# Kernel tuning notes

Hardware: AMD Instinct MI355X
Metric: run time of the kernel (lower is better)

The kernel has to match this reference:

```python
import jax, jax.numpy as jnp
import numpy as np
import math

N_COMP = 8          # config.project.shape[1]
REG_TOPK = 4        # config.reg_topk
PROJ_MAX = 7.0      # config.project = linspace(0, 7, 8)
ACC = PROJ_MAX / (N_COMP - 1)  # = 1.0


def _conv(x, w, b, pad):
    y = jax.lax.conv_general_dilated(
        x, w, window_strides=(1, 1), padding=[(pad, pad), (pad, pad)],
        dimension_numbers=("NCHW", "OIHW", "NCHW"))
    return y + b[None, :, None, None]


def setup_inputs() -> dict:
    key = jax.random.key(0)
    ks = jax.random.split(key, 16)
    std = 0.01
    f32 = jnp.float32
    feature = jax.random.normal(ks[0], (8, 256, 100, 152), dtype=f32)
    cls_w = jax.random.normal(ks[1], (4, 256, 256, 3, 3), dtype=f32) * std
    cls_b = jnp.zeros((4, 256), dtype=f32)
    box_w = jax.random.normal(ks[2], (4, 256, 256, 3, 3), dtype=f32) * std
    box_b = jnp.zeros((4, 256), dtype=f32)
    score_w = jax.random.normal(ks[3], (1, 256, 3, 3), dtype=f32) * std
    score_b = jnp.full((1,), -math.log((1 - 0.01) / 0.01), dtype=f32)
    pred_w = jax.random.normal(ks[4], (64, 256, 3, 3), dtype=f32) * std
    pred_b = jnp.zeros((64,), dtype=f32)
    ctn_w = jax.random.normal(ks[5], (1, 256, 3, 3), dtype=f32) * std
    ctn_b = jnp.zeros((1,), dtype=f32)
    conf_w1 = jax.random.normal(ks[6], (64, 48, 1, 1), dtype=f32) * std
    conf_b1 = jnp.zeros((64,), dtype=f32)
    conf_w2 = jax.random.normal(ks[7], (1, 64, 1, 1), dtype=f32) * std
    conf_b2 = jnp.zeros((1,), dtype=f32)
    return dict(feature=feature, cls_w=cls_w, cls_b=cls_b, box_w=box_w, box_b=box_b,
                score_w=score_w, score_b=score_b, pred_w=pred_w, pred_b=pred_b,
                ctn_w=ctn_w, ctn_b=ctn_b, conf_w1=conf_w1, conf_b1=conf_b1,
                conf_w2=conf_w2, conf_b2=conf_b2)


def reference(feature, cls_w, cls_b, box_w, box_b, score_w, score_b,
              pred_w, pred_b, ctn_w, ctn_b, conf_w1, conf_b1, conf_w2, conf_b2):
    x = feature
    for i in range(4):
        x = jax.nn.relu(_conv(x, cls_w[i], cls_b[i], 1))
    cls_score = _conv(x, score_w, score_b, 1)          # (N,1,H,W)
    # bbox subnet
    y = feature
    for i in range(4):
        y = jax.nn.relu(_conv(y, box_w[i], box_b[i], 1))
    bbox_pred = _conv(y, pred_w, pred_b, 1)            # (N,64,H,W)
    ctn = _conv(y, ctn_w, ctn_b, 1)                    # (N,1,H,W)

    N, C, H, W = bbox_pred.shape
    # rows = N*H*W*4 (4 box sides), 16 = 2*n_component per side
    flat = bbox_pred.transpose(0, 2, 3, 1).reshape(-1, 2 * N_COMP)
    logit = flat[:, :N_COMP]
    lstd = flat[:, N_COMP:]
    prob = jax.nn.softmax(logit, axis=1)               # (rows, n)
    sigma = jnp.exp(lstd)                              # (rows, n)
    proj = jnp.arange(N_COMP, dtype=flat.dtype) * ACC  # linspace(0, 7, 8)
    inv = 1.0 / (sigma * jnp.asarray(np.sqrt(2.0), flat.dtype))  # (rows, n)
    # Normal(mean=proj_i, std=sigma_i).cdf(proj_j +/- acc)
    diff = proj[None, None, :] - proj[None, :, None]   # (1, n_i, n_j) = z_j - mean_i
    cdf_hi = 0.5 * (1.0 + jax.lax.erf((diff + ACC) * inv[:, :, None]))
    cdf_lo = 0.5 * (1.0 + jax.lax.erf((diff - ACC) * inv[:, :, None]))
    pmf = jnp.sum((cdf_hi - cdf_lo) * prob[:, :, None], axis=1)  # (rows, n)

    toppmf, idx = jax.lax.top_k(pmf, REG_TOPK)         # (rows, k)
    toplstd = jnp.take_along_axis(lstd, idx, axis=1)
    topprob = jnp.take_along_axis(prob, idx, axis=1)

    def tochw(t):  # (rows,k) -> (N, 4*k, H, W)
        return t.reshape(N, H, W, -1).transpose(0, 3, 1, 2)

    stat = jnp.concatenate([tochw(toplstd), tochw(topprob), tochw(toppmf)], axis=1)  # (N,48,H,W)
    h = jax.nn.relu(_conv(stat, conf_w1, conf_b1, 0))
    quality = jax.nn.sigmoid(_conv(h, conf_w2, conf_b2, 0))  # (N,1,H,W)

    cls_out = jax.nn.sigmoid(cls_score) * quality
    pred_cls = cls_out.transpose(0, 2, 3, 1).reshape(N, -1, 1)
    pred_reg = bbox_pred.transpose(0, 2, 3, 1).reshape(N, -1, 4 * 2 * N_COMP)
    pred_ctn = ctn.transpose(0, 2, 3, 1).reshape(N, -1, 1)
    return (pred_cls, pred_reg, pred_ctn)
```

## Files before the change

kernel.cpp:

```cpp
#include <hip/hip_runtime.h>

typedef unsigned short u16;
typedef _Float16 f16;
typedef __attribute__((ext_vector_type(4))) float f32x4;
typedef __attribute__((ext_vector_type(8))) _Float16 f16x8;
typedef __attribute__((ext_vector_type(8))) unsigned short u16x8;

#define NIMG 8
#define HH 100
#define WW 152
#define HP 102
#define WP 154
#define NPIX (NIMG*HH*WW)
#define ACT_ELEMS ((size_t)NIMG*HP*WP*256)
#define ACT_BYTES (ACT_ELEMS*2)

__device__ __forceinline__ u16 f2h(float x){
    f16 h = (f16)x;
    return __builtin_bit_cast(u16, h);
}

__device__ __forceinline__ void g2l16(const u16* g, u16* l){
    __builtin_amdgcn_global_load_lds((const __attribute__((address_space(1))) unsigned int*)g,
                                     (__attribute__((address_space(3))) unsigned int*)l, 16, 0, 0);
}

__global__ void zero_borders(u16* A, u16* B, u16* C, u16* D){
    int id = blockIdx.x*256 + threadIdx.x;
    int ch = id & 31; int t = id >> 5;
    int pb = t % 508; int nimg = t / 508;
    int hp, wp;
    if (pb < 154)      { hp = 0;            wp = pb; }
    else if (pb < 308) { hp = 101;          wp = pb - 154; }
    else if (pb < 408) { hp = pb - 308 + 1; wp = 0; }
    else               { hp = pb - 408 + 1; wp = 153; }
    size_t off = ((size_t)((nimg*HP + hp)*WP + wp))*256 + ch*8;
    u16x8 z = {};
    *(u16x8*)(A+off) = z; *(u16x8*)(B+off) = z;
    *(u16x8*)(C+off) = z; *(u16x8*)(D+off) = z;
}

__global__ void feat2act(const float* __restrict__ F, u16* __restrict__ D1, u16* __restrict__ D2){
    __shared__ float t[64][65];
    int bid = blockIdx.x;
    int wb = bid % 3; bid /= 3;
    int cb = bid & 3; bid >>= 2;
    int h = bid % 100; int nimg = bid / 100;
    int c0 = cb*64, w0 = wb*64;
    int tid = threadIdx.x;
    int cl = tid >> 6;
    int wl = tid & 63;
    #pragma unroll
    for (int rr=0; rr<16; ++rr){
        int c = rr*4 + cl;
        int w = w0 + wl;
        float v = 0.f;
        if (w < WW) v = F[ ((size_t)((nimg*256 + c0 + c)*HH + h))*WW + w ];
        t[c][wl] = v;
    }
    __syncthreads();
    int wl2 = tid >> 6;
    int cl2 = tid & 63;
    #pragma unroll
    for (int rr=0; rr<16; ++rr){
        int w = rr*4 + wl2;
        if (w0 + w < WW){
            u16 h16 = f2h(t[cl2][w]);
            size_t dst = ((size_t)((nimg*HP + h + 1)*WP + (w0 + w + 1)))*256 + c0 + cl2;
            D1[dst] = h16;
            D2[dst] = h16;
        }
    }
}

__global__ void wt_tower(const float* __restrict__ srcC, const float* __restrict__ srcB,
                         u16* __restrict__ dC, u16* __restrict__ dB){
    int gidx = blockIdx.x*256 + threadIdx.x;
    const int HALF = 4*9*256*256;
    const float* src = (gidx < HALF) ? srcC : srcB;
    u16* d           = (gidx < HALF) ? dC : dB;
    int idx = (gidx < HALF) ? gidx : gidx - HALF;
    int ci = idx & 255; int t = idx >> 8;
    int co = t & 255; t >>= 8;
    int tap = t % 9; int l = t / 9;
    d[idx] = f2h(src[ ((size_t)((l*256+co)*256+ci))*9 + tap ]);
}
__global__ void wt_predctn(const float* __restrict__ pw, const float* __restrict__ cw,
                           u16* __restrict__ d){
    int idx = blockIdx.x*256 + threadIdx.x;
    int ci = idx & 255; int co = (idx>>8) & 127; int tap = idx >> 15;
    float v = 0.f;
    if (co < 64)       v = pw[ ((size_t)(co*256+ci))*9 + tap ];
    else if (co == 64) v = cw[ (size_t)ci*9 + tap ];
    d[idx] = f2h(v);
}
__global__ void wt_score(const float* __restrict__ sw, u16* __restrict__ d){
    int idx = blockIdx.x*256 + threadIdx.x;
    int ci = idx & 255; int co = (idx>>8) & 127; int tap = idx >> 15;
    d[idx] = f2h((co == 0) ? sw[ (size_t)ci*9 + tap ] : 0.f);
}
__global__ void prep_bias(const float* pb, const float* cb, const float* sb, float* bpc, float* bsc){
    int i = threadIdx.x;
    bpc[i] = (i < 64) ? pb[i] : ((i == 64) ? cb[0] : 0.f);
    bsc[i] = (i == 0) ? sb[0] : 0.f;
}

template<int MODE>
__global__ __launch_bounds__(256, 2) void conv3x3_k(
    const u16* __restrict__ Ain0, const u16* __restrict__ Ain1,
    const u16* __restrict__ W0,  const u16* __restrict__ W1,
    const float* __restrict__ bias0, const float* __restrict__ bias1,
    u16* __restrict__ Oh0, u16* __restrict__ Oh1,
    float* __restrict__ O1, float* __restrict__ O2,
    int nPerTower, int NB, int COUTP)
{
    constexpr int MR = (MODE==0) ? 4 : 2;
    constexpr int NR = (MODE==0) ? 4 : ((MODE==1) ? 5 : 1);

    __shared__ u16 lds[32768];
    const int tid  = threadIdx.x;
    const int lane = tid & 63;
    const int wave = tid >> 6;

    int nwg = gridDim.x;
    int bid = blockIdx.x;
    int qq  = nwg >> 3;
    int swz = (bid & 7)*qq + (bid >> 3);
    int tower = (swz >= nPerTower) ? 1 : 0;
    int id = swz - tower*nPerTower;

    const u16* Ain    = tower ? Ain1  : Ain0;
    const u16* W      = tower ? W1    : W0;
    const float* bias = tower ? bias1 : bias0;
    u16* Oh           = tower ? Oh1   : Oh0;

    int nblk = id % NB;
    int mblk = id / NB;
    int nimg = mblk / 125;
    int rem  = mblk - nimg*125;
    int ht   = rem / 5;
    int wt5  = rem - ht*5;
    int h0 = ht*4, w0 = wt5*32;
    int co0 = nblk*128;

    int aoff[4], boff[4];
    #pragma unroll
    for (int it=0; it<4; ++it){
        int s = it*256 + tid;
        int p = s >> 3, ch = s & 7;
        int chs = ch ^ (p & 7);
        int i = p >> 5, j = p & 31;
        aoff[it] = ((nimg*HP + h0 + i)*WP + (w0 + j))*256 + chs*8;
        boff[it] = (co0 + p)*256 + chs*8;
    }
    const int ldst = wave*512;

    const int r  = lane & 15;
    const int q4 = lane >> 4;
    const int c0k = ((q4    ) ^ (r & 7)) * 8;
    const int c1k = ((q4 + 4) ^ (r & 7)) * 8;
    int wm, wn;
    if (MODE == 0){ wm = wave >> 1; wn = wave & 1; } else { wm = wave; wn = 0; }
    const int aBase = (wm*(MR*16) + r)*64;
    const int bBase = 8192 + (wn*64 + r)*64;

    f32x4 acc[MR][NR];
    #pragma unroll
    for (int m=0;m<MR;m++)
        #pragma unroll
        for (int n=0;n<NR;n++)
            acc[m][n] = (f32x4)0.0f;

    auto stage = [&](int t, int b){
        int tap = t >> 2, kb = t & 3;
        int kh = tap/3, kw = tap - kh*3;
        int adel = (kh*WP + kw)*256 + kb*64;
        int bdel = tap*COUTP*256 + kb*64;
        u16* L = lds + b*16384;
        #pragma unroll
        for (int it=0; it<4; ++it)
            g2l16(Ain + aoff[it] + adel, L +        it*2048 + ldst);
        #pragma unroll
        for (int it=0; it<4; ++it)
            g2l16(W + bdel + boff[it], L + 8192 + it*2048 + ldst);
    };

    stage(0, 0);
    stage(1, 1);
    asm volatile("s_waitcnt vmcnt(8)" ::: "memory");
    __builtin_amdgcn_s_barrier();

    for (int t=0; t<36; ++t){
        int b = t & 1;
        const u16* L = lds + b*16384;
        f16x8 a0[MR], a1[MR], b0[NR], b1[NR];
        #pragma unroll
        for (int m=0;m<MR;m++){
            a0[m] = *(const f16x8*)(L + aBase + m*1024 + c0k);
            a1[m] = *(const f16x8*)(L + aBase + m*1024 + c1k);
        }
        #pragma unroll
        for (int n=0;n<NR;n++){
            b0[n] = *(const f16x8*)(L + bBase + n*1024 + c0k);
            b1[n] = *(const f16x8*)(L + bBase + n*1024 + c1k);
        }
        asm volatile("s_waitcnt lgkmcnt(0)" ::: "memory");
        __builtin_amdgcn_s_barrier();
        __builtin_amdgcn_sched_barrier(0);
        if (t < 34) stage(t+2, b);
        __builtin_amdgcn_s_setprio(1);
        #pragma unroll
        for (int n=0;n<NR;n++){
            #pragma unroll
            for (int m=0;m<MR;m++){
                acc[m][n] = __builtin_amdgcn_mfma_f32_16x16x32_f16(a0[m], b0[n], acc[m][n], 0,0,0);
                acc[m][n] = __builtin_amdgcn_mfma_f32_16x16x32_f16(a1[m], b1[n], acc[m][n], 0,0,0);
            }
        }
        __builtin_amdgcn_s_setprio(0);
        __builtin_amdgcn_sched_barrier(0);
        if (t < 34) { asm volatile("s_waitcnt vmcnt(8)" ::: "memory"); }
        else        { asm volatile("s_waitcnt vmcnt(0)" ::: "memory"); }
        __builtin_amdgcn_s_barrier();
    }

    float bcol[NR];
    #pragma unroll
    for (int n=0;n<NR;n++) bcol[n] = bias[co0 + wn*64 + n*16 + r];

    if (MODE == 0){
        #pragma unroll
        for (int m=0;m<MR;m++)
            #pragma unroll
            for (int n=0;n<NR;n++)
                #pragma unroll
                for (int jj=0;jj<4;jj++){
                    float v = fmaxf(acc[m][n][jj] + bcol[n], 0.f);
                    int p = wm*64 + m*16 + q4*4 + jj;
                    int c = wn*64 + n*16 + r;
                    lds[p*128 + c] = f2h(v);
                }
        __syncthreads();
        #pragma unroll
        for (int it=0; it<8; ++it){
            int s = it*256 + tid;
            int p = s >> 4, chh = s & 15;
            int i = p >> 5, j = p & 31;
            if (w0 + j < WW){
                size_t dst = ((size_t)((nimg*HP + h0 + i + 1)*WP + (w0 + j + 1)))*256 + co0 + chh*8;
                *(u16x8*)(Oh + dst) = *(const u16x8*)(lds + p*128 + chh*8);
            }
        }
    } else {
        #pragma unroll
        for (int m=0;m<MR;m++)
            #pragma unroll
            for (int n=0;n<NR;n++)
                #pragma unroll
                for (int jj=0;jj<4;jj++){
                    float v = acc[m][n][jj] + bcol[n];
                    int p = wm*32 + m*16 + q4*4 + jj;
                    int c = n*16 + r;
                    int i = p >> 5, j = p & 31;
                    if (w0 + j < WW){
                        int pix = nimg*(HH*WW) + (h0+i)*WW + (w0+j);
                        if (MODE == 1){
                            if (c < 64)       O1[(size_t)pix*64 + c] = v;
                            else if (c == 64) O2[pix] = v;
                        } else {
                            if (c == 0) O1[pix] = v;
                        }
                    }
                }
    }
}

__global__ __launch_bounds__(256) void fuse_stat(
    const float* __restrict__ bbox, const float* __restrict__ cls_score,
    const float* __restrict__ w1, const float* __restrict__ b1,
    const float* __restrict__ w2, const float* __restrict__ b2,
    float* __restrict__ pred_cls)
{
    __shared__ float sstat[48][256];
    int tid = threadIdx.x;
    int pix = blockIdx.x*256 + tid;
    if (pix >= NPIX) return;
    const f32x4* row4 = (const f32x4*)(bbox + (size_t)pix*64);
    for (int g=0; g<4; ++g){
        f32x4 v0 = row4[g*4+0], v1 = row4[g*4+1], v2 = row4[g*4+2], v3 = row4[g*4+3];
        float lg[8], ls[8];
        #pragma unroll
        for (int k=0;k<4;k++){ lg[k]=v0[k]; lg[4+k]=v1[k]; ls[k]=v2[k]; ls[4+k]=v3[k]; }
        float m = lg[0];
        #pragma unroll
        for (int k=1;k<8;k++) m = fmaxf(m, lg[k]);
        float e[8], s = 0.f;
        #pragma unroll
        for (int k=0;k<8;k++){ e[k] = expf(lg[k]-m); s += e[k]; }
        float isum = 1.0f/s;
        float prob[8];
        #pragma unroll
        for (int k=0;k<8;k++) prob[k] = e[k]*isum;
        float pmf[8];
        #pragma unroll
        for (int k=0;k<8;k++) pmf[k] = 0.f;
        #pragma unroll
        for (int i=0;i<8;i++){
            float invi = 1.0f/(expf(ls[i]) * 1.41421356237309515f);
            float pi = prob[i];
            #pragma unroll
            for (int j=0;j<8;j++){
                float d = (float)(j - i);
                pmf[j] = fmaf(0.5f*(erff((d+1.0f)*invi) - erff((d-1.0f)*invi)), pi, pmf[j]);
            }
        }
        int used = 0;
        #pragma unroll
        for (int t=0;t<4;t++){
            float bv = -3.0e38f; int bi = 0;
            #pragma unroll
            for (int j=0;j<8;j++){
                bool ok = (((used>>j)&1)==0) && (pmf[j] > bv);
                bv = ok ? pmf[j] : bv;
                bi = ok ? j : bi;
            }
            used |= (1<<bi);
            float sl=0.f, sp=0.f;
            #pragma unroll
            for (int j=0;j<8;j++){ if (j==bi){ sl=ls[j]; sp=prob[j]; } }
            sstat[g*4+t][tid]    = sl;
            sstat[16+g*4+t][tid] = sp;
            sstat[32+g*4+t][tid] = bv;
        }
    }
    float q = b2[0];
    for (int u=0; u<64; ++u){
        float h = b1[u];
        #pragma unroll
        for (int c=0;c<48;c++) h = fmaf(sstat[c][tid], w1[u*48+c], h);
        q = fmaf(fmaxf(h,0.f), w2[u], q);
    }
    float quality = 1.0f/(1.0f+expf(-q));
    float cs = cls_score[pix];
    pred_cls[pix] = quality/(1.0f+expf(-cs));
}

extern "C" void kernel_launch(void* const* d_in, const int* in_sizes, int n_in,
                              void* d_out, int out_size, void* d_ws, size_t ws_size,
                              hipStream_t stream) {
    (void)in_sizes; (void)n_in; (void)out_size;
    const float* feature = (const float*)d_in[0];
    const float* cls_w   = (const float*)d_in[1];
    const float* cls_b   = (const float*)d_in[2];
    const float* box_w   = (const float*)d_in[3];
    const float* box_b   = (const float*)d_in[4];
    const float* score_w = (const float*)d_in[5];
    const float* score_b = (const float*)d_in[6];
    const float* pred_w  = (const float*)d_in[7];
    const float* pred_b  = (const float*)d_in[8];
    const float* ctn_w   = (const float*)d_in[9];
    const float* ctn_b   = (const float*)d_in[10];
    const float* conf_w1 = (const float*)d_in[11];
    const float* conf_b1 = (const float*)d_in[12];
    const float* conf_w2 = (const float*)d_in[13];
    const float* conf_b2 = (const float*)d_in[14];

    float* out      = (float*)d_out;
    float* pred_cls = out;
    float* pred_reg = out + NPIX;
    float* pred_ctn = out + NPIX + (size_t)NPIX*64;

    char* ws = (char*)d_ws;
    size_t off = 0;
    auto alloc = [&](size_t b){ size_t rr = off; off += (b + 255) & ~(size_t)255; return rr; };
    u16* aA = (u16*)(ws + alloc(ACT_BYTES + 65536));
    u16* aB = (u16*)(ws + alloc(ACT_BYTES + 65536));
    u16* aC = (u16*)(ws + alloc(ACT_BYTES + 65536));
    u16* aD = (u16*)(ws + alloc(ACT_BYTES + 65536));
    const size_t TWR = (size_t)4*9*256*256;
    const size_t HDW = (size_t)9*128*256;
    u16* wCls = (u16*)(ws + alloc(TWR*2));
    u16* wBox = (u16*)(ws + alloc(TWR*2));
    u16* wSc  = (u16*)(ws + alloc(HDW*2));
    u16* wPc  = (u16*)(ws + alloc(HDW*2));
    float* bPc = (float*)(ws + alloc(128*4));
    float* bSc = (float*)(ws + alloc(128*4));
    float* clsScore = (float*)(ws + alloc((size_t)NPIX*4));
    if (ws_size < off) return;

    dim3 B(256);
    zero_borders<<<508, B, 0, stream>>>(aA, aB, aC, aD);
    wt_tower<<<18432, B, 0, stream>>>(cls_w, box_w, wCls, wBox);
    wt_score<<<1152, B, 0, stream>>>(score_w, wSc);
    wt_predctn<<<1152, B, 0, stream>>>(pred_w, ctn_w, wPc);
    prep_bias<<<1, 128, 0, stream>>>(pred_b, ctn_b, score_b, bPc, bSc);

    const size_t LW = (size_t)9*256*256;
    feat2act<<<9600, B, 0, stream>>>(feature, aA, aC);
    conv3x3_k<0><<<4000, B, 0, stream>>>(aA, aC, wCls+0*LW, wBox+0*LW, cls_b+0*256, box_b+0*256, aB, aD, nullptr, nullptr, 2000, 2, 256);
    conv3x3_k<0><<<4000, B, 0, stream>>>(aB, aD, wCls+1*LW, wBox+1*LW, cls_b+1*256, box_b+1*256, aA, aC, nullptr, nullptr, 2000, 2, 256);
    conv3x3_k<0><<<4000, B, 0, stream>>>(aA, aC, wCls+2*LW, wBox+2*LW, cls_b+2*256, box_b+2*256, aB, aD, nullptr, nullptr, 2000, 2, 256);
    conv3x3_k<0><<<4000, B, 0, stream>>>(aB, aD, wCls+3*LW, wBox+3*LW, cls_b+3*256, box_b+3*256, aA, aC, nullptr, nullptr, 2000, 2, 256);
    conv3x3_k<2><<<1000, B, 0, stream>>>(aA, aA, wSc, wSc, bSc, bSc, nullptr, nullptr, clsScore, nullptr, 1000, 1, 128);
    conv3x3_k<1><<<1000, B, 0, stream>>>(aC, aC, wPc, wPc, bPc, bPc, nullptr, nullptr, pred_reg, pred_ctn, 1000, 1, 128);
    fuse_stat<<<475, B, 0, stream>>>(pred_reg, clsScore, conf_w1, conf_b1, conf_w2, conf_b2, pred_cls);
}
```

Baseline: 1.357 ms.

## Use 256x256 output tiles with 512-thread blocks for tower convolutions

Replaces the 128x128-tile tower conv kernel with a new kernel that has 8 waves and computes 256 pixels by all 256 output channels per block. Each A and B load is reused across twice as many MFMAs, so global and LDS traffic per FLOP drops. The k-step is split into four phases that interleave LDS reads, prefetch of the next stage and MFMAs. The 8-row tiles run past the image edge (100 rows is not a multiple of 8), which costs some wasted compute on clamped rows. The larger 128 KB LDS footprint and higher register use may limit occupancy, and the head convs are simplified to single-tower versions.

```diff
diff --git a/kernel.cpp b/kernel.cpp
--- a/kernel.cpp
+++ b/kernel.cpp
@@ -105,17 +105,227 @@
     bsc[i] = (i == 0) ? sb[0] : 0.f;
 }
 
-template<int MODE>
-__global__ __launch_bounds__(256, 2) void conv3x3_k(
+__global__ __launch_bounds__(512, 2) void conv_tower8(
     const u16* __restrict__ Ain0, const u16* __restrict__ Ain1,
     const u16* __restrict__ W0,  const u16* __restrict__ W1,
     const float* __restrict__ bias0, const float* __restrict__ bias1,
-    u16* __restrict__ Oh0, u16* __restrict__ Oh1,
-    float* __restrict__ O1, float* __restrict__ O2,
-    int nPerTower, int NB, int COUTP)
+    u16* __restrict__ Oh0, u16* __restrict__ Oh1)
 {
-    constexpr int MR = (MODE==0) ? 4 : 2;
-    constexpr int NR = (MODE==0) ? 4 : ((MODE==1) ? 5 : 1);
+    __shared__ u16 lds[65536];
+    const int tid  = threadIdx.x;
+    const int lane = tid & 63;
+    const int wave = tid >> 6;
+
+    int nwg = gridDim.x;
+    int bid = blockIdx.x;
+    int qq  = nwg >> 3;
+    int swz = (bid & 7)*qq + (bid >> 3);
+    int tower = (swz >= 520) ? 1 : 0;
+    int id = swz - tower*520;
+
+    const u16* Ain    = tower ? Ain1  : Ain0;
+    const u16* W      = tower ? W1    : W0;
+    const float* bias = tower ? bias1 : bias0;
+    u16* Oh           = tower ? Oh1   : Oh0;
+
+    int nimg = id / 65;
+    int rem  = id - nimg*65;
+    int ht   = rem / 5;
+    int wt5  = rem - ht*5;
+    int h0 = ht*8, w0 = wt5*32;
+
+    int aoff[2][2], boff[2][2];
+    #pragma unroll
+    for (int h=0; h<2; ++h)
+        #pragma unroll
+        for (int it=0; it<2; ++it){
+            int s = it*512 + tid;
+            int p = s >> 3, ch = s & 7;
+            int chs = ch ^ (p & 7);
+            int g = h*128 + p;
+            int i = g >> 5, j = g & 31;
+            int row = h0 + i; if (row > 99)  row = 99;
+            int col = w0 + j; if (col > 151) col = 151;
+            aoff[h][it] = ((nimg*HP + row)*WP + col)*256 + chs*8;
+            boff[h][it] = (h*128 + p)*256 + chs*8;
+        }
+    const int wofs = wave*512;
+
+    const int r  = lane & 15;
+    const int q4 = lane >> 4;
+    const int rk = r & 7;
+    const int wm = wave >> 2;
+    const int wn = wave & 3;
+    const int aRdB = (wm*128 + r)*64 + (q4 ^ rk)*8;
+    const int bRdB = 16384 + (wn*64 + r)*64 + (q4 ^ rk)*8;
+
+    f32x4 acc[8][4];
+    #pragma unroll
+    for (int m=0;m<8;m++)
+        #pragma unroll
+        for (int n=0;n<4;n++)
+            acc[m][n] = (f32x4)0.0f;
+
+    auto stageA = [&](int tt, int buf){
+        int tap = tt >> 2, kb = tt & 3;
+        int kh = tap/3, kw = tap - kh*3;
+        int adel = (kh*WP + kw)*256 + kb*64;
+        u16* L = lds + buf*32768;
+        #pragma unroll
+        for (int h=0; h<2; ++h)
+            #pragma unroll
+            for (int it=0; it<2; ++it)
+                g2l16(Ain + aoff[h][it] + adel, L + h*8192 + it*4096 + wofs);
+    };
+    auto stageB = [&](int tt, int buf){
+        int tap = tt >> 2, kb = tt & 3;
+        int bdel = tap*65536 + kb*64;
+        u16* L = lds + buf*32768 + 16384;
+        #pragma unroll
+        for (int h=0; h<2; ++h)
+            #pragma unroll
+            for (int it=0; it<2; ++it)
+                g2l16(W + bdel + boff[h][it], L + h*8192 + it*4096 + wofs);
+    };
+
+    stageA(0, 0); stageB(0, 0);
+    stageA(1, 1); stageB(1, 1);
+    asm volatile("s_waitcnt vmcnt(8)" ::: "memory");
+    __builtin_amdgcn_s_barrier();
+
+    #pragma unroll 1
+    for (int t=0; t<36; ++t){
+        const int cur = t & 1;
+        const u16* L = lds + cur*32768;
+        const bool pre = (t < 34);
+
+        f16x8 aL0[4], aL1[4], bL0[2], bL1[2];
+        #pragma unroll
+        for (int m=0;m<4;m++){
+            aL0[m] = *(const f16x8*)(L + (aRdB + m*1024));
+            aL1[m] = *(const f16x8*)(L + ((aRdB + m*1024) ^ 32));
+        }
+        #pragma unroll
+        for (int n=0;n<2;n++){
+            bL0[n] = *(const f16x8*)(L + (bRdB + n*1024));
+            bL1[n] = *(const f16x8*)(L + ((bRdB + n*1024) ^ 32));
+        }
+        __builtin_amdgcn_s_barrier();
+        asm volatile("s_waitcnt lgkmcnt(0)" ::: "memory");
+        __builtin_amdgcn_sched_barrier(0);
+        __builtin_amdgcn_s_setprio(1);
+        #pragma unroll
+        for (int n=0;n<2;n++)
+            #pragma unroll
+            for (int m=0;m<4;m++){
+                acc[m][n] = __builtin_amdgcn_mfma_f32_16x16x32_f16(aL0[m], bL0[n], acc[m][n], 0,0,0);
+                acc[m][n] = __builtin_amdgcn_mfma_f32_16x16x32_f16(aL1[m], bL1[n], acc[m][n], 0,0,0);
+            }
+        __builtin_amdgcn_s_setprio(0);
+        __builtin_amdgcn_s_barrier();
+
+        f16x8 bH0[2], bH1[2];
+        #pragma unroll
+        for (int n=0;n<2;n++){
+            bH0[n] = *(const f16x8*)(L + (bRdB + (n+2)*1024));
+            bH1[n] = *(const f16x8*)(L + ((bRdB + (n+2)*1024) ^ 32));
+        }
+        __builtin_amdgcn_s_barrier();
+        asm volatile("s_waitcnt lgkmcnt(0)" ::: "memory");
+        __builtin_amdgcn_sched_barrier(0);
+        __builtin_amdgcn_s_setprio(1);
+        #pragma unroll
+        for (int n=0;n<2;n++)
+            #pragma unroll
+            for (int m=0;m<4;m++){
+                acc[m][n+2] = __builtin_amdgcn_mfma_f32_16x16x32_f16(aL0[m], bH0[n], acc[m][n+2], 0,0,0);
+                acc[m][n+2] = __builtin_amdgcn_mfma_f32_16x16x32_f16(aL1[m], bH1[n], acc[m][n+2], 0,0,0);
+            }
+        __builtin_amdgcn_s_setprio(0);
+        __builtin_amdgcn_s_barrier();
+
+        f16x8 aH0[4], aH1[4];
+        #pragma unroll
+        for (int m=0;m<4;m++){
+            aH0[m] = *(const f16x8*)(L + (aRdB + (m+4)*1024));
+            aH1[m] = *(const f16x8*)(L + ((aRdB + (m+4)*1024) ^ 32));
+        }
+        if (pre) stageB(t+2, cur);
+        __builtin_amdgcn_s_barrier();
+        asm volatile("s_waitcnt lgkmcnt(0)" ::: "memory");
+        __builtin_amdgcn_sched_barrier(0);
+        __builtin_amdgcn_s_setprio(1);
+        #pragma unroll
+        for (int n=0;n<2;n++)
+            #pragma unroll
+            for (int m=0;m<4;m++){
+                acc[m+4][n] = __builtin_amdgcn_mfma_f32_16x16x32_f16(aH0[m], bL0[n], acc[m+4][n], 0,0,0);
+                acc[m+4][n] = __builtin_amdgcn_mfma_f32_16x16x32_f16(aH1[m], bL1[n], acc[m+4][n], 0,0,0);
+            }
+        __builtin_amdgcn_s_setprio(0);
+        __builtin_amdgcn_s_barrier();
+
+        if (pre) stageA(t+2, cur);
+        __builtin_amdgcn_s_barrier();
+        __builtin_amdgcn_sched_barrier(0);
+        __builtin_amdgcn_s_setprio(1);
+        #pragma unroll
+        for (int n=0;n<2;n++)
+            #pragma unroll
+            for (int m=0;m<4;m++){
+                acc[m+4][n+2] = __builtin_amdgcn_mfma_f32_16x16x32_f16(aH0[m], bH0[n], acc[m+4][n+2], 0,0,0);
+                acc[m+4][n+2] = __builtin_amdgcn_mfma_f32_16x16x32_f16(aH1[m], bH1[n], acc[m+4][n+2], 0,0,0);
+            }
+        __builtin_amdgcn_s_setprio(0);
+        __builtin_amdgcn_sched_barrier(0);
+        if (pre) { asm volatile("s_waitcnt vmcnt(8)" ::: "memory"); }
+        else     { asm volatile("s_waitcnt vmcnt(0)" ::: "memory"); }
+        __builtin_amdgcn_s_barrier();
+    }
+
+    float bcol[4];
+    #pragma unroll
+    for (int n=0;n<4;n++) bcol[n] = bias[wn*64 + n*16 + r];
+
+    #pragma unroll
+    for (int P=0; P<2; ++P){
+        if (P) __syncthreads();
+        if (wm == P){
+            #pragma unroll
+            for (int m=0;m<8;m++)
+                #pragma unroll
+                for (int n=0;n<4;n++)
+                    #pragma unroll
+                    for (int jj=0;jj<4;jj++){
+                        float v = fmaxf(acc[m][n][jj] + bcol[n], 0.f);
+                        int px = m*16 + q4*4 + jj;
+                        int c  = wn*64 + n*16 + r;
+                        lds[px*264 + c] = f2h(v);
+                    }
+        }
+        __syncthreads();
+        #pragma unroll
+        for (int it=0; it<8; ++it){
+            int s = it*512 + tid;
+            int lr = s >> 5, chh = s & 31;
+            int g = P*128 + lr;
+            int i = g >> 5, j = g & 31;
+            if (h0 + i < HH && w0 + j < WW){
+                size_t dst = ((size_t)((nimg*HP + h0 + i + 1)*WP + (w0 + j + 1)))*256 + chh*8;
+                *(u16x8*)(Oh + dst) = *(const u16x8*)(lds + lr*264 + chh*8);
+            }
+        }
+    }
+}
+
+template<int MODE>
+__global__ __launch_bounds__(256, 2) void conv3x3_k(
+    const u16* __restrict__ Ain, const u16* __restrict__ W,
+    const float* __restrict__ bias,
+    float* __restrict__ O1, float* __restrict__ O2, int COUTP)
+{
+    constexpr int MR = 2;
+    constexpr int NR = (MODE==1) ? 5 : 1;
 
     __shared__ u16 lds[32768];
     const int tid  = threadIdx.x;
@@ -126,22 +336,12 @@
     int bid = blockIdx.x;
     int qq  = nwg >> 3;
     int swz = (bid & 7)*qq + (bid >> 3);
-    int tower = (swz >= nPerTower) ? 1 : 0;
-    int id = swz - tower*nPerTower;
-
-    const u16* Ain    = tower ? Ain1  : Ain0;
-    const u16* W      = tower ? W1    : W0;
-    const float* bias = tower ? bias1 : bias0;
-    u16* Oh           = tower ? Oh1   : Oh0;
-
-    int nblk = id % NB;
-    int mblk = id / NB;
+    int mblk = swz;
     int nimg = mblk / 125;
     int rem  = mblk - nimg*125;
     int ht   = rem / 5;
     int wt5  = rem - ht*5;
     int h0 = ht*4, w0 = wt5*32;
-    int co0 = nblk*128;
 
     int aoff[4], boff[4];
     #pragma unroll
@@ -151,7 +351,7 @@
         int chs = ch ^ (p & 7);
         int i = p >> 5, j = p & 31;
         aoff[it] = ((nimg*HP + h0 + i)*WP + (w0 + j))*256 + chs*8;
-        boff[it] = (co0 + p)*256 + chs*8;
+        boff[it] = p*256 + chs*8;
     }
     const int ldst = wave*512;
 
@@ -159,10 +359,9 @@
     const int q4 = lane >> 4;
     const int c0k = ((q4    ) ^ (r & 7)) * 8;
     const int c1k = ((q4 + 4) ^ (r & 7)) * 8;
-    int wm, wn;
-    if (MODE == 0){ wm = wave >> 1; wn = wave & 1; } else { wm = wave; wn = 0; }
+    const int wm = wave;
     const int aBase = (wm*(MR*16) + r)*64;
-    const int bBase = 8192 + (wn*64 + r)*64;
+    const int bBase = 8192 + r*64;
 
     f32x4 acc[MR][NR];
     #pragma unroll
@@ -210,13 +409,12 @@
         if (t < 34) stage(t+2, b);
         __builtin_amdgcn_s_setprio(1);
         #pragma unroll
-        for (int n=0;n<NR;n++){
+        for (int n=0;n<NR;n++)
             #pragma unroll
             for (int m=0;m<MR;m++){
                 acc[m][n] = __builtin_amdgcn_mfma_f32_16x16x32_f16(a0[m], b0[n], acc[m][n], 0,0,0);
                 acc[m][n] = __builtin_amdgcn_mfma_f32_16x16x32_f16(a1[m], b1[n], acc[m][n], 0,0,0);
             }
-        }
         __builtin_amdgcn_s_setprio(0);
         __builtin_amdgcn_sched_barrier(0);
         if (t < 34) { asm volatile("s_waitcnt vmcnt(8)" ::: "memory"); }
@@ -226,53 +424,28 @@
 
     float bcol[NR];
     #pragma unroll
-    for (int n=0;n<NR;n++) bcol[n] = bias[co0 + wn*64 + n*16 + r];
-
-    if (MODE == 0){
-        #pragma unroll
-        for (int m=0;m<MR;m++)
-            #pragma unroll
-            for (int n=0;n<NR;n++)
-                #pragma unroll
-                for (int jj=0;jj<4;jj++){
-                    float v = fmaxf(acc[m][n][jj] + bcol[n], 0.f);
-                    int p = wm*64 + m*16 + q4*4 + jj;
-                    int c = wn*64 + n*16 + r;
-                    lds[p*128 + c] = f2h(v);
-                }
-        __syncthreads();
-        #pragma unroll
-        for (int it=0; it<8; ++it){
-            int s = it*256 + tid;
-            int p = s >> 4, chh = s & 15;
-            int i = p >> 5, j = p & 31;
-            if (w0 + j < WW){
-                size_t dst = ((size_t)((nimg*HP + h0 + i + 1)*WP + (w0 + j + 1)))*256 + co0 + chh*8;
-                *(u16x8*)(Oh + dst) = *(const u16x8*)(lds + p*128 + chh*8);
-            }
-        }
-    } else {
-        #pragma unroll
-        for (int m=0;m<MR;m++)
-            #pragma unroll
-            for (int n=0;n<NR;n++)
-                #pragma unroll
-                for (int jj=0;jj<4;jj++){
-                    float v = acc[m][n][jj] + bcol[n];
-                    int p = wm*32 + m*16 + q4*4 + jj;
-                    int c = n*16 + r;
-                    int i = p >> 5, j = p & 31;
-                    if (w0 + j < WW){
-                        int pix = nimg*(HH*WW) + (h0+i)*WW + (w0+j);
-                        if (MODE == 1){
-                            if (c < 64)       O1[(size_t)pix*64 + c] = v;
-                            else if (c == 64) O2[pix] = v;
-                        } else {
-                            if (c == 0) O1[pix] = v;
-                        }
+    for (int n=0;n<NR;n++) bcol[n] = bias[n*16 + r];
+
+    #pragma unroll
+    for (int m=0;m<MR;m++)
+        #pragma unroll
+        for (int n=0;n<NR;n++)
+            #pragma unroll
+            for (int jj=0;jj<4;jj++){
+                float v = acc[m][n][jj] + bcol[n];
+                int p = wm*32 + m*16 + q4*4 + jj;
+                int c = n*16 + r;
+                int i = p >> 5, j = p & 31;
+                if (w0 + j < WW){
+                    int pix = nimg*(HH*WW) + (h0+i)*WW + (w0+j);
+                    if (MODE == 1){
+                        if (c < 64)       O1[(size_t)pix*64 + c] = v;
+                        else if (c == 64) O2[pix] = v;
+                    } else {
+                        if (c == 0) O1[pix] = v;
                     }
                 }
-    }
+            }
 }
 
 __global__ __launch_bounds__(256) void fuse_stat(
@@ -397,11 +570,12 @@
 
     const size_t LW = (size_t)9*256*256;
     feat2act<<<9600, B, 0, stream>>>(feature, aA, aC);
-    conv3x3_k<0><<<4000, B, 0, stream>>>(aA, aC, wCls+0*LW, wBox+0*LW, cls_b+0*256, box_b+0*256, aB, aD, nullptr, nullptr, 2000, 2, 256);
-    conv3x3_k<0><<<4000, B, 0, stream>>>(aB, aD, wCls+1*LW, wBox+1*LW, cls_b+1*256, box_b+1*256, aA, aC, nullptr, nullptr, 2000, 2, 256);
-    conv3x3_k<0><<<4000, B, 0, stream>>>(aA, aC, wCls+2*LW, wBox+2*LW, cls_b+2*256, box_b+2*256, aB, aD, nullptr, nullptr, 2000, 2, 256);
-    conv3x3_k<0><<<4000, B, 0, stream>>>(aB, aD, wCls+3*LW, wBox+3*LW, cls_b+3*256, box_b+3*256, aA, aC, nullptr, nullptr, 2000, 2, 256);
-    conv3x3_k<2><<<1000, B, 0, stream>>>(aA, aA, wSc, wSc, bSc, bSc, nullptr, nullptr, clsScore, nullptr, 1000, 1, 128);
-    conv3x3_k<1><<<1000, B, 0, stream>>>(aC, aC, wPc, wPc, bPc, bPc, nullptr, nullptr, pred_reg, pred_ctn, 1000, 1, 128);
+    dim3 TB(512);
+    conv_tower8<<<1040, TB, 0, stream>>>(aA, aC, wCls+0*LW, wBox+0*LW, cls_b+0*256, box_b+0*256, aB, aD);
+    conv_tower8<<<1040, TB, 0, stream>>>(aB, aD, wCls+1*LW, wBox+1*LW, cls_b+1*256, box_b+1*256, aA, aC);
+    conv_tower8<<<1040, TB, 0, stream>>>(aA, aC, wCls+2*LW, wBox+2*LW, cls_b+2*256, box_b+2*256, aB, aD);
+    conv_tower8<<<1040, TB, 0, stream>>>(aB, aD, wCls+3*LW, wBox+3*LW, cls_b+3*256, box_b+3*256, aA, aC);
+    conv3x3_k<2><<<1000, B, 0, stream>>>(aA, wSc, bSc, clsScore, nullptr, 128);
+    conv3x3_k<1><<<1000, B, 0, stream>>>(aC, wPc, bPc, pred_reg, pred_ctn, 128);
     fuse_stat<<<475, B, 0, stream>>>(pred_reg, clsScore, conf_w1, conf_b1, conf_w2, conf_b2, pred_cls);
 }
```

New measurement: 1.605 ms. 1.18x slower.

## Widen tower conv tile to all 256 output channels with 32-wide K steps

Applied to the files above, without the earlier changes.

Adds a dedicated tower conv kernel in which each workgroup computes all 256 output channels for a 128-pixel tile, instead of two 128-channel blocks. This halves the number of times each activation tile is reloaded. The K step drops to 32 channels per stage (72 stages) with a new XOR swizzle, and each wave holds a 4x8 accumulator array. The epilogue writes results back through LDS in two passes. The trade-off is higher register pressure from 128 accumulator floats per thread, and more barriers per output from the shorter K steps.

```diff
diff --git a/kernel.cpp b/kernel.cpp
--- a/kernel.cpp
+++ b/kernel.cpp
@@ -105,17 +105,165 @@
     bsc[i] = (i == 0) ? sb[0] : 0.f;
 }
 
-template<int MODE>
-__global__ __launch_bounds__(256, 2) void conv3x3_k(
+__global__ __launch_bounds__(256, 2) void conv_tower(
     const u16* __restrict__ Ain0, const u16* __restrict__ Ain1,
     const u16* __restrict__ W0,  const u16* __restrict__ W1,
     const float* __restrict__ bias0, const float* __restrict__ bias1,
-    u16* __restrict__ Oh0, u16* __restrict__ Oh1,
-    float* __restrict__ O1, float* __restrict__ O2,
-    int nPerTower, int NB, int COUTP)
+    u16* __restrict__ Oh0, u16* __restrict__ Oh1)
 {
-    constexpr int MR = (MODE==0) ? 4 : 2;
-    constexpr int NR = (MODE==0) ? 4 : ((MODE==1) ? 5 : 1);
+    __shared__ u16 lds[33792];
+    const int tid  = threadIdx.x;
+    const int lane = tid & 63;
+    const int wave = tid >> 6;
+
+    int nwg = gridDim.x;
+    int bid = blockIdx.x;
+    int qq  = nwg >> 3;
+    int swz = (bid & 7)*qq + (bid >> 3);
+    int tower = (swz >= 1000) ? 1 : 0;
+    int id = swz - tower*1000;
+
+    const u16* Ain    = tower ? Ain1  : Ain0;
+    const u16* W      = tower ? W1    : W0;
+    const float* bias = tower ? bias1 : bias0;
+    u16* Oh           = tower ? Oh1   : Oh0;
+
+    int nimg = id / 125;
+    int rem  = id - nimg*125;
+    int ht   = rem / 5;
+    int wt5  = rem - ht*5;
+    int h0 = ht*4, w0 = wt5*32;
+
+    int aoff[2];
+    #pragma unroll
+    for (int it=0; it<2; ++it){
+        int s = it*256 + tid;
+        int p = s >> 2, ch = s & 3;
+        int chs = ch ^ ((p + (p >> 2)) & 3);
+        int i = p >> 5, j = p & 31;
+        aoff[it] = ((nimg*HP + h0 + i)*WP + (w0 + j))*256 + chs*8;
+    }
+    int boff[4];
+    #pragma unroll
+    for (int it=0; it<4; ++it){
+        int s = it*256 + tid;
+        int p = s >> 2, ch = s & 3;
+        int chs = ch ^ ((p + (p >> 2)) & 3);
+        boff[it] = p*256 + chs*8;
+    }
+    const int ldst = wave*512;
+
+    const int r  = lane & 15;
+    const int q4 = lane >> 4;
+    const int wm = wave >> 1, wn = wave & 1;
+    int aRd[4];
+    #pragma unroll
+    for (int m=0;m<4;m++){
+        int row = wm*64 + m*16 + r;
+        aRd[m] = row*32 + ((q4 ^ ((row + (row>>2)) & 3)))*8;
+    }
+    int bRd[8];
+    #pragma unroll
+    for (int n=0;n<8;n++){
+        int row = wn*128 + n*16 + r;
+        bRd[n] = 4096 + row*32 + ((q4 ^ ((row + (row>>2)) & 3)))*8;
+    }
+
+    f32x4 acc[4][8];
+    #pragma unroll
+    for (int m=0;m<4;m++)
+        #pragma unroll
+        for (int n=0;n<8;n++)
+            acc[m][n] = (f32x4)0.0f;
+
+    auto stage = [&](int t, int b){
+        int tap = t >> 3, kb = t & 7;
+        int kh = tap/3, kw = tap - kh*3;
+        int adel = (kh*WP + kw)*256 + kb*32;
+        int bdel = tap*65536 + kb*32;
+        u16* L = lds + b*12288;
+        #pragma unroll
+        for (int it=0; it<2; ++it)
+            g2l16(Ain + aoff[it] + adel, L +        it*2048 + ldst);
+        #pragma unroll
+        for (int it=0; it<4; ++it)
+            g2l16(W + bdel + boff[it], L + 4096 + it*2048 + ldst);
+    };
+
+    stage(0, 0);
+    stage(1, 1);
+    asm volatile("s_waitcnt vmcnt(6)" ::: "memory");
+    __builtin_amdgcn_s_barrier();
+
+    #pragma unroll 1
+    for (int t=0; t<72; ++t){
+        int b = t & 1;
+        const u16* L = lds + b*12288;
+        f16x8 af[4], bf[8];
+        #pragma unroll
+        for (int m=0;m<4;m++) af[m] = *(const f16x8*)(L + aRd[m]);
+        #pragma unroll
+        for (int n=0;n<8;n++) bf[n] = *(const f16x8*)(L + bRd[n]);
+        asm volatile("s_waitcnt lgkmcnt(0)" ::: "memory");
+        __builtin_amdgcn_s_barrier();
+        __builtin_amdgcn_sched_barrier(0);
+        if (t < 70) stage(t+2, b);
+        __builtin_amdgcn_s_setprio(1);
+        #pragma unroll
+        for (int n=0;n<8;n++)
+            #pragma unroll
+            for (int m=0;m<4;m++)
+                acc[m][n] = __builtin_amdgcn_mfma_f32_16x16x32_f16(af[m], bf[n], acc[m][n], 0,0,0);
+        __builtin_amdgcn_s_setprio(0);
+        __builtin_amdgcn_sched_barrier(0);
+        if (t < 70) { asm volatile("s_waitcnt vmcnt(6)" ::: "memory"); }
+        else        { asm volatile("s_waitcnt vmcnt(0)" ::: "memory"); }
+        __builtin_amdgcn_s_barrier();
+    }
+
+    float bcol[8];
+    #pragma unroll
+    for (int n=0;n<8;n++) bcol[n] = bias[wn*128 + n*16 + r];
+
+    #pragma unroll
+    for (int P=0; P<2; ++P){
+        __syncthreads();
+        if (wm == P){
+            #pragma unroll
+            for (int m=0;m<4;m++)
+                #pragma unroll
+                for (int n=0;n<8;n++)
+                    #pragma unroll
+                    for (int jj=0;jj<4;jj++){
+                        float v = fmaxf(acc[m][n][jj] + bcol[n], 0.f);
+                        int px = m*16 + q4*4 + jj;
+                        int c  = wn*128 + n*16 + r;
+                        lds[px*264 + c] = f2h(v);
+                    }
+        }
+        __syncthreads();
+        #pragma unroll
+        for (int it=0; it<8; ++it){
+            int s = it*256 + tid;
+            int lr = s >> 5, chh = s & 31;
+            int g = P*64 + lr;
+            int i = g >> 5, j = g & 31;
+            if (w0 + j < WW){
+                size_t dst = ((size_t)((nimg*HP + h0 + i + 1)*WP + (w0 + j + 1)))*256 + chh*8;
+                *(u16x8*)(Oh + dst) = *(const u16x8*)(lds + lr*264 + chh*8);
+            }
+        }
+    }
+}
+
+template<int MODE>
+__global__ __launch_bounds__(256, 2) void conv3x3_k(
+    const u16* __restrict__ Ain, const u16* __restrict__ W,
+    const float* __restrict__ bias,
+    float* __restrict__ O1, float* __restrict__ O2, int COUTP)
+{
+    constexpr int MR = 2;
+    constexpr int NR = (MODE==1) ? 5 : 1;
 
     __shared__ u16 lds[32768];
     const int tid  = threadIdx.x;
@@ -126,22 +274,12 @@
     int bid = blockIdx.x;
     int qq  = nwg >> 3;
     int swz = (bid & 7)*qq + (bid >> 3);
-    int tower = (swz >= nPerTower) ? 1 : 0;
-    int id = swz - tower*nPerTower;
-
-    const u16* Ain    = tower ? Ain1  : Ain0;
-    const u16* W      = tower ? W1    : W0;
-    const float* bias = tower ? bias1 : bias0;
-    u16* Oh           = tower ? Oh1   : Oh0;
-
-    int nblk = id % NB;
-    int mblk = id / NB;
+    int mblk = swz;
     int nimg = mblk / 125;
     int rem  = mblk - nimg*125;
     int ht   = rem / 5;
     int wt5  = rem - ht*5;
     int h0 = ht*4, w0 = wt5*32;
-    int co0 = nblk*128;
 
     int aoff[4], boff[4];
     #pragma unroll
@@ -151,7 +289,7 @@
         int chs = ch ^ (p & 7);
         int i = p >> 5, j = p & 31;
         aoff[it] = ((nimg*HP + h0 + i)*WP + (w0 + j))*256 + chs*8;
-        boff[it] = (co0 + p)*256 + chs*8;
+        boff[it] = p*256 + chs*8;
     }
     const int ldst = wave*512;
 
@@ -159,10 +297,9 @@
     const int q4 = lane >> 4;
     const int c0k = ((q4    ) ^ (r & 7)) * 8;
     const int c1k = ((q4 + 4) ^ (r & 7)) * 8;
-    int wm, wn;
-    if (MODE == 0){ wm = wave >> 1; wn = wave & 1; } else { wm = wave; wn = 0; }
+    const int wm = wave;
     const int aBase = (wm*(MR*16) + r)*64;
-    const int bBase = 8192 + (wn*64 + r)*64;
+    const int bBase = 8192 + r*64;
 
     f32x4 acc[MR][NR];
     #pragma unroll
@@ -210,13 +347,12 @@
         if (t < 34) stage(t+2, b);
         __builtin_amdgcn_s_setprio(1);
         #pragma unroll
-        for (int n=0;n<NR;n++){
+        for (int n=0;n<NR;n++)
             #pragma unroll
             for (int m=0;m<MR;m++){
                 acc[m][n] = __builtin_amdgcn_mfma_f32_16x16x32_f16(a0[m], b0[n], acc[m][n], 0,0,0);
                 acc[m][n] = __builtin_amdgcn_mfma_f32_16x16x32_f16(a1[m], b1[n], acc[m][n], 0,0,0);
             }
-        }
         __builtin_amdgcn_s_setprio(0);
         __builtin_amdgcn_sched_barrier(0);
         if (t < 34) { asm volatile("s_waitcnt vmcnt(8)" ::: "memory"); }
@@ -226,53 +362,28 @@
 
     float bcol[NR];
     #pragma unroll
-    for (int n=0;n<NR;n++) bcol[n] = bias[co0 + wn*64 + n*16 + r];
-
-    if (MODE == 0){
-        #pragma unroll
-        for (int m=0;m<MR;m++)
-            #pragma unroll
-            for (int n=0;n<NR;n++)
-                #pragma unroll
-                for (int jj=0;jj<4;jj++){
-                    float v = fmaxf(acc[m][n][jj] + bcol[n], 0.f);
-                    int p = wm*64 + m*16 + q4*4 + jj;
-                    int c = wn*64 + n*16 + r;
-                    lds[p*128 + c] = f2h(v);
-                }
-        __syncthreads();
-        #pragma unroll
-        for (int it=0; it<8; ++it){
-            int s = it*256 + tid;
-            int p = s >> 4, chh = s & 15;
-            int i = p >> 5, j = p & 31;
-            if (w0 + j < WW){
-                size_t dst = ((size_t)((nimg*HP + h0 + i + 1)*WP + (w0 + j + 1)))*256 + co0 + chh*8;
-                *(u16x8*)(Oh + dst) = *(const u16x8*)(lds + p*128 + chh*8);
-            }
-        }
-    } else {
-        #pragma unroll
-        for (int m=0;m<MR;m++)
-            #pragma unroll
-            for (int n=0;n<NR;n++)
-                #pragma unroll
-                for (int jj=0;jj<4;jj++){
-                    float v = acc[m][n][jj] + bcol[n];
-                    int p = wm*32 + m*16 + q4*4 + jj;
-                    int c = n*16 + r;
-                    int i = p >> 5, j = p & 31;
-                    if (w0 + j < WW){
-                        int pix = nimg*(HH*WW) + (h0+i)*WW + (w0+j);
-                        if (MODE == 1){
-                            if (c < 64)       O1[(size_t)pix*64 + c] = v;
-                            else if (c == 64) O2[pix] = v;
-                        } else {
-                            if (c == 0) O1[pix] = v;
-                        }
+    for (int n=0;n<NR;n++) bcol[n] = bias[n*16 + r];
+
+    #pragma unroll
+    for (int m=0;m<MR;m++)
+        #pragma unroll
+        for (int n=0;n<NR;n++)
+            #pragma unroll
+            for (int jj=0;jj<4;jj++){
+                float v = acc[m][n][jj] + bcol[n];
+                int p = wm*32 + m*16 + q4*4 + jj;
+                int c = n*16 + r;
+                int i = p >> 5, j = p & 31;
+                if (w0 + j < WW){
+                    int pix = nimg*(HH*WW) + (h0+i)*WW + (w0+j);
+                    if (MODE == 1){
+                        if (c < 64)       O1[(size_t)pix*64 + c] = v;
+                        else if (c == 64) O2[pix] = v;
+                    } else {
+                        if (c == 0) O1[pix] = v;
                     }
                 }
-    }
+            }
 }
 
 __global__ __launch_bounds__(256) void fuse_stat(
@@ -397,11 +508,11 @@
 
     const size_t LW = (size_t)9*256*256;
     feat2act<<<9600, B, 0, stream>>>(feature, aA, aC);
-    conv3x3_k<0><<<4000, B, 0, stream>>>(aA, aC, wCls+0*LW, wBox+0*LW, cls_b+0*256, box_b+0*256, aB, aD, nullptr, nullptr, 2000, 2, 256);
-    conv3x3_k<0><<<4000, B, 0, stream>>>(aB, aD, wCls+1*LW, wBox+1*LW, cls_b+1*256, box_b+1*256, aA, aC, nullptr, nullptr, 2000, 2, 256);
-    conv3x3_k<0><<<4000, B, 0, stream>>>(aA, aC, wCls+2*LW, wBox+2*LW, cls_b+2*256, box_b+2*256, aB, aD, nullptr, nullptr, 2000, 2, 256);
-    conv3x3_k<0><<<4000, B, 0, stream>>>(aB, aD, wCls+3*LW, wBox+3*LW, cls_b+3*256, box_b+3*256, aA, aC, nullptr, nullptr, 2000, 2, 256);
-    conv3x3_k<2><<<1000, B, 0, stream>>>(aA, aA, wSc, wSc, bSc, bSc, nullptr, nullptr, clsScore, nullptr, 1000, 1, 128);
-    conv3x3_k<1><<<1000, B, 0, stream>>>(aC, aC, wPc, wPc, bPc, bPc, nullptr, nullptr, pred_reg, pred_ctn, 1000, 1, 128);
+    conv_tower<<<2000, B, 0, stream>>>(aA, aC, wCls+0*LW, wBox+0*LW, cls_b+0*256, box_b+0*256, aB, aD);
+    conv_tower<<<2000, B, 0, stream>>>(aB, aD, wCls+1*LW, wBox+1*LW, cls_b+1*256, box_b+1*256, aA, aC);
+    conv_tower<<<2000, B, 0, stream>>>(aA, aC, wCls+2*LW, wBox+2*LW, cls_b+2*256, box_b+2*256, aB, aD);
+    conv_tower<<<2000, B, 0, stream>>>(aB, aD, wCls+3*LW, wBox+3*LW, cls_b+3*256, box_b+3*256, aA, aC);
+    conv3x3_k<2><<<1000, B, 0, stream>>>(aA, wSc, bSc, clsScore, nullptr, 128);
+    conv3x3_k<1><<<1000, B, 0, stream>>>(aC, wPc, bPc, pred_reg, pred_ctn, 128);
     fuse_stat<<<475, B, 0, stream>>>(pred_reg, clsScore, conf_w1, conf_b1, conf_w2, conf_b2, pred_cls);
 }
```

Result: slower. 1.428 ms (+5.3%).
